# Kernel tuning notes

Hardware: AMD Instinct MI355X
Metric: run time of the kernel (lower is better)

Reference implementation:

```python
import jax, jax.numpy as jnp
import numpy as np

DIM = 2048
HEADS = 16
HEAD_DIM = DIM // HEADS
EPS = 1e-5


def layernorm(x, g, b):
    mu = jnp.mean(x, axis=-1, keepdims=True)
    var = jnp.mean(jnp.square(x - mu), axis=-1, keepdims=True)
    return (x - mu) * jax.lax.rsqrt(var + EPS) * g + b


def bitlinear(x, w):
    # BitNet b1.58: per-tensor ternary weight quant + per-token int8 absmax activation quant
    ws = jnp.clip(jnp.mean(jnp.abs(w)), 1e-5, None)          # weight scale (mean |w|)
    wq = jnp.clip(jnp.round(w / ws), -1.0, 1.0) * ws          # ternary {-1,0,1}*ws
    xs = 127.0 / jnp.clip(jnp.max(jnp.abs(x), axis=-1, keepdims=True), 1e-5, None)
    xq = jnp.clip(jnp.round(x * xs), -128.0, 127.0) / xs      # int8 absmax, dequantized
    return jnp.einsum('bnc,oc->bno', xq, wq)


def attention(x, w_qkv, w_proj):
    B, N, C = x.shape
    qkv = bitlinear(x, w_qkv).reshape(B, N, 3, HEADS, HEAD_DIM)
    q, k, v = [qkv[:, :, i].transpose(0, 2, 1, 3) for i in range(3)]  # [B,H,N,D]
    scores = jnp.einsum('bhqd,bhkd->bhqk', q, k) / jnp.sqrt(jnp.asarray(HEAD_DIM, x.dtype))
    attn = jax.nn.softmax(scores, axis=-1)
    o = jnp.einsum('bhqk,bhkd->bhqd', attn, v)
    o = o.transpose(0, 2, 1, 3).reshape(B, N, C)
    return bitlinear(o, w_proj)


def setup_inputs() -> dict:
    key = jax.random.key(0)
    ks = jax.random.split(key, 9)
    s = 0.02
    return {
        'x': jax.random.normal(ks[0], (2, 2048, DIM), dtype=jnp.float32),
        'w_qkv': jax.random.normal(ks[1], (3 * DIM, DIM), dtype=jnp.float32) * s,
        'w_proj': jax.random.normal(ks[2], (DIM, DIM), dtype=jnp.float32) * s,
        'w_fc1': jax.random.normal(ks[3], (4 * DIM, DIM), dtype=jnp.float32) * s,
        'w_fc2': jax.random.normal(ks[4], (DIM, 4 * DIM), dtype=jnp.float32) * s,
        'g1': jnp.ones((DIM,), jnp.float32),
        'b1': jnp.zeros((DIM,), jnp.float32),
        'g2': jnp.ones((DIM,), jnp.float32),
        'b2': jnp.zeros((DIM,), jnp.float32),
    }


def reference(x, w_qkv, w_proj, w_fc1, w_fc2, g1, b1, g2, b2):
    x = x + attention(layernorm(x, g1, b1), w_qkv, w_proj)
    h = bitlinear(layernorm(x, g2, b2), w_fc1)
    h = jax.nn.gelu(h, approximate=False)
    h = bitlinear(h, w_fc2)
    return x + h
```

## Files before the change

kernel.cpp:

```cpp
#include <hip/hip_runtime.h>
#include <cstdint>

#define DEVI __device__ __forceinline__

typedef int v4i __attribute__((ext_vector_type(4)));
typedef short v8s __attribute__((ext_vector_type(8)));
typedef float v4f __attribute__((ext_vector_type(4)));

DEVI float bf_lo(unsigned u) { return __uint_as_float(u << 16); }
DEVI float bf_hi(unsigned u) { return __uint_as_float(u & 0xffff0000u); }
DEVI float bf2f(unsigned short h) { return __uint_as_float(((unsigned)h) << 16); }
DEVI unsigned short f2bf(float f) {
  unsigned u = __float_as_uint(f);
  u += 0x7fffu + ((u >> 16) & 1u);
  return (unsigned short)(u >> 16);
}

DEVI void async_copy16(void* l, const void* g) {
  __builtin_amdgcn_global_load_lds((const __attribute__((address_space(1))) void*)g,
                                   (__attribute__((address_space(3))) void*)l,
                                   16, 0, 0);
}

DEVI float wave_sum(float v) {
#pragma unroll
  for (int o = 32; o > 0; o >>= 1) v += __shfl_xor(v, o, 64);
  return v;
}
DEVI float wave_max(float v) {
#pragma unroll
  for (int o = 32; o > 0; o >>= 1) v = fmaxf(v, __shfl_xor(v, o, 64));
  return v;
}

__global__ __launch_bounds__(256) void absum_kernel(const float* __restrict__ w, long n,
                                                    float* __restrict__ acc) {
  long stride = (long)gridDim.x * 1024;
  float s = 0.f;
  for (long i = ((long)blockIdx.x * 256 + threadIdx.x) * 4; i < n; i += stride) {
    float4 v = *(const float4*)(w + i);
    s += fabsf(v.x) + fabsf(v.y) + fabsf(v.z) + fabsf(v.w);
  }
  s = wave_sum(s);
  __shared__ float sc[4];
  int tid = threadIdx.x;
  if ((tid & 63) == 0) sc[tid >> 6] = s;
  __syncthreads();
  if (tid == 0) atomicAdd(acc, sc[0] + sc[1] + sc[2] + sc[3]);
}

__global__ __launch_bounds__(256) void wquant_kernel(const float* __restrict__ w, long n4,
                                                     const float* __restrict__ acc, float cnt,
                                                     signed char* __restrict__ out) {
  float wsv = fmaxf(acc[0] / cnt, 1e-5f);
  float inv = 1.0f / wsv;
  long stride = (long)gridDim.x * 256;
  for (long i = (long)blockIdx.x * 256 + threadIdx.x; i < n4; i += stride) {
    float4 v = *(const float4*)(w + i * 4);
    int q0 = max(-1, min(1, (int)rintf(v.x * inv)));
    int q1 = max(-1, min(1, (int)rintf(v.y * inv)));
    int q2 = max(-1, min(1, (int)rintf(v.z * inv)));
    int q3 = max(-1, min(1, (int)rintf(v.w * inv)));
    unsigned r = (q0 & 0xff) | ((q1 & 0xff) << 8) | ((q2 & 0xff) << 16) | ((q3 & 0xff) << 24);
    ((unsigned*)out)[i] = r;
  }
}

__global__ __launch_bounds__(256) void ln_quant_kernel(const float* __restrict__ x,
                                                       const float* __restrict__ g,
                                                       const float* __restrict__ b,
                                                       signed char* __restrict__ q,
                                                       float* __restrict__ inv_s) {
  int row = blockIdx.x, tid = threadIdx.x;
  const float4* xr = (const float4*)(x + (long)row * 2048);
  float4 a0 = xr[tid * 2], a1 = xr[tid * 2 + 1];
  float xv[8] = {a0.x, a0.y, a0.z, a0.w, a1.x, a1.y, a1.z, a1.w};
  float s = 0.f, s2 = 0.f;
#pragma unroll
  for (int e = 0; e < 8; ++e) { s += xv[e]; s2 += xv[e] * xv[e]; }
  s = wave_sum(s); s2 = wave_sum(s2);
  __shared__ float sc[8];
  if ((tid & 63) == 0) { sc[tid >> 6] = s; sc[4 + (tid >> 6)] = s2; }
  __syncthreads();
  float mean = (sc[0] + sc[1] + sc[2] + sc[3]) * (1.f / 2048.f);
  float var = (sc[4] + sc[5] + sc[6] + sc[7]) * (1.f / 2048.f) - mean * mean;
  float rs = 1.0f / sqrtf(var + 1e-5f);
  float4 g0 = ((const float4*)g)[tid * 2], g1v = ((const float4*)g)[tid * 2 + 1];
  float4 b0 = ((const float4*)b)[tid * 2], b1v = ((const float4*)b)[tid * 2 + 1];
  float gv[8] = {g0.x, g0.y, g0.z, g0.w, g1v.x, g1v.y, g1v.z, g1v.w};
  float bv[8] = {b0.x, b0.y, b0.z, b0.w, b1v.x, b1v.y, b1v.z, b1v.w};
  float y[8];
  float am = 0.f;
#pragma unroll
  for (int e = 0; e < 8; ++e) {
    y[e] = (xv[e] - mean) * rs * gv[e] + bv[e];
    am = fmaxf(am, fabsf(y[e]));
  }
  am = wave_max(am);
  __syncthreads();
  if ((tid & 63) == 0) sc[tid >> 6] = am;
  __syncthreads();
  am = fmaxf(fmaxf(sc[0], sc[1]), fmaxf(sc[2], sc[3]));
  float c = fmaxf(am, 1e-5f);
  float xs = 127.0f / c;
  union { signed char c8[8]; int2 v; } u;
#pragma unroll
  for (int e = 0; e < 8; ++e) {
    int t = (int)rintf(y[e] * xs);
    u.c8[e] = (signed char)max(-128, min(127, t));
  }
  ((int2*)(q + (long)row * 2048))[tid] = u.v;
  if (tid == 0) inv_s[row] = c * (1.0f / 127.0f);
}

template <int R>
__global__ __launch_bounds__(256) void row_quant_kernel(const unsigned short* __restrict__ in,
                                                        signed char* __restrict__ q,
                                                        float* __restrict__ inv_s) {
  constexpr int V = R / 2048;
  int row = blockIdx.x, tid = threadIdx.x;
  const uint4* p = (const uint4*)(in + (long)row * R);
  float y[V * 8];
  float am = 0.f;
#pragma unroll
  for (int v = 0; v < V; ++v) {
    uint4 d = p[tid * V + v];
    unsigned xw[4] = {d.x, d.y, d.z, d.w};
#pragma unroll
    for (int k = 0; k < 4; ++k) {
      y[v * 8 + k * 2] = bf_lo(xw[k]);
      y[v * 8 + k * 2 + 1] = bf_hi(xw[k]);
    }
  }
#pragma unroll
  for (int e = 0; e < V * 8; ++e) am = fmaxf(am, fabsf(y[e]));
  am = wave_max(am);
  __shared__ float sc[4];
  if ((tid & 63) == 0) sc[tid >> 6] = am;
  __syncthreads();
  am = fmaxf(fmaxf(sc[0], sc[1]), fmaxf(sc[2], sc[3]));
  float c = fmaxf(am, 1e-5f);
  float xs = 127.0f / c;
  signed char* qr = q + (long)row * R;
#pragma unroll
  for (int v = 0; v < V; ++v) {
    union { signed char c8[8]; long l; } u;
#pragma unroll
    for (int k = 0; k < 8; ++k) {
      int t = (int)rintf(y[v * 8 + k] * xs);
      u.c8[k] = (signed char)max(-128, min(127, t));
    }
    ((long*)qr)[tid * V + v] = u.l;
  }
  if (tid == 0) inv_s[row] = c * (1.0f / 127.0f);
}

template <int EPI>
__global__ __launch_bounds__(256)
void gemm_i8(const signed char* __restrict__ A, const signed char* __restrict__ B,
             int N, int K, const float* __restrict__ wacc, float wcount,
             const float* __restrict__ inv_s, const float* __restrict__ res,
             void* __restrict__ outp) {
  __shared__ signed char As[128 * 64];
  __shared__ signed char Bs[128 * 64];
  int tid = threadIdx.x;
  int m0 = blockIdx.y * 128, n0 = blockIdx.x * 128;
  int w = tid >> 6, lane = tid & 63;
  int wm = (w >> 1) * 64, wn = (w & 1) * 64;
  int lr = lane & 15, lk = (lane >> 4) * 16;

  v4i acc[4][4] = {};

  int u0 = w * 128 + lane;
  int u1 = u0 + 64;
  const signed char* ga0 = A + (long)(m0 + (u0 >> 2)) * K + (u0 & 3) * 16;
  const signed char* ga1 = A + (long)(m0 + (u1 >> 2)) * K + (u1 & 3) * 16;
  const signed char* gb0 = B + (long)(n0 + (u0 >> 2)) * K + (u0 & 3) * 16;
  const signed char* gb1 = B + (long)(n0 + (u1 >> 2)) * K + (u1 & 3) * 16;
  char* la0 = (char*)As + (w * 128) * 16;
  char* la1 = (char*)As + (w * 128 + 64) * 16;
  char* lb0 = (char*)Bs + (w * 128) * 16;
  char* lb1 = (char*)Bs + (w * 128 + 64) * 16;

  for (int kk = 0; kk < K; kk += 64) {
    async_copy16(la0, ga0 + kk);
    async_copy16(la1, ga1 + kk);
    async_copy16(lb0, gb0 + kk);
    async_copy16(lb1, gb1 + kk);
    __syncthreads();
    v4i af[4], bf[4];
#pragma unroll
    for (int t = 0; t < 4; ++t) af[t] = *(const v4i*)(As + (wm + t * 16 + lr) * 64 + lk);
#pragma unroll
    for (int t = 0; t < 4; ++t) bf[t] = *(const v4i*)(Bs + (wn + t * 16 + lr) * 64 + lk);
#pragma unroll
    for (int i = 0; i < 4; ++i)
#pragma unroll
      for (int j = 0; j < 4; ++j)
        acc[i][j] = __builtin_amdgcn_mfma_i32_16x16x64_i8(af[i], bf[j], acc[i][j], 0, 0, 0);
    __syncthreads();
  }

  float wsv = fmaxf(wacc[0] / wcount, 1e-5f);
#pragma unroll
  for (int i = 0; i < 4; ++i) {
    int rowbase = m0 + wm + i * 16 + (lane >> 4) * 4;
#pragma unroll
    for (int r = 0; r < 4; ++r) {
      int row = rowbase + r;
      float s = wsv * inv_s[row];
#pragma unroll
      for (int j = 0; j < 4; ++j) {
        int col = n0 + wn + j * 16 + (lane & 15);
        long off = (long)row * N + col;
        float v = (float)acc[i][j][r] * s;
        if constexpr (EPI == 0) {
          ((unsigned short*)outp)[off] = f2bf(v);
        } else if constexpr (EPI == 1) {
          ((float*)outp)[off] = v + res[off];
        } else {
          float gvv = 0.5f * v * (1.0f + erff(v * 0.70710678118654752f));
          ((unsigned short*)outp)[off] = f2bf(gvv);
        }
      }
    }
  }
}

__global__ __launch_bounds__(256, 2)
void fattn_kernel(const unsigned short* __restrict__ qkv, unsigned short* __restrict__ o) {
  constexpr int VROW = 72;
  constexpr int PROW = 72;
  __shared__ char Ks[16384];
  __shared__ unsigned short Vt[128 * VROW];
  __shared__ unsigned short Ps[4 * 32 * PROW];

  int tid = threadIdx.x;
  int w = tid >> 6, lane = tid & 63;
  int l = lane & 15, q = lane >> 4;
  int qt = blockIdx.x, bh = blockIdx.y;
  int bb = bh >> 4, hh = bh & 15;
  const unsigned short* base = qkv + (long)bb * 2048 * 6144;
  int q0 = qt * 128;

  v8s aq[2][4];
#pragma unroll
  for (int s = 0; s < 2; ++s) {
    const unsigned short* qrow = base + (long)(q0 + w * 32 + s * 16 + l) * 6144 + hh * 128;
#pragma unroll
    for (int kf = 0; kf < 4; ++kf) aq[s][kf] = *(const v8s*)(qrow + kf * 32 + q * 8);
  }

  v4f oacc[2][8];
#pragma unroll
  for (int s = 0; s < 2; ++s)
#pragma unroll
    for (int t = 0; t < 8; ++t) oacc[s][t] = (v4f){0.f, 0.f, 0.f, 0.f};
  float mrow[2][4], lrow[2][4];
#pragma unroll
  for (int s = 0; s < 2; ++s)
#pragma unroll
    for (int r = 0; r < 4; ++r) { mrow[s][r] = -1e30f; lrow[s][r] = 0.f; }

  unsigned short* pw = Ps + w * 32 * PROW;
  const unsigned short* kbase_g = base + 2048 + hh * 128;
  const unsigned short* vbase_g = base + 4096 + hh * 128;
  int kg = tid & 7, dg = tid >> 3;
  constexpr float SC = 0.08838834764831845f;

  for (int kt = 0; kt < 32; ++kt) {
    int k0 = kt * 64;
#pragma unroll
    for (int i = 0; i < 4; ++i) {
      int c = i * 256 + w * 64 + lane;
      int key = c >> 4;
      int dch = (c & 15) ^ (key & 15);
      async_copy16(Ks + (i * 256 + w * 64) * 16,
                   kbase_g + (long)(k0 + key) * 6144 + dch * 8);
    }
    {
      uint2 lv[8];
#pragma unroll
      for (int i = 0; i < 8; ++i)
        lv[i] = *(const uint2*)(vbase_g + (long)(k0 + kg * 8 + i) * 6144 + dg * 4);
#pragma unroll
      for (int jd = 0; jd < 4; ++jd) {
        v8s pk;
#pragma unroll
        for (int i = 0; i < 8; ++i) {
          unsigned word = (jd < 2) ? lv[i].x : lv[i].y;
          pk[i] = (short)((jd & 1) ? (word >> 16) : (word & 0xffffu));
        }
        *(v8s*)(Vt + (dg * 4 + jd) * VROW + kg * 8) = pk;
      }
    }
    __syncthreads();

    v4f sacc[2][4];
#pragma unroll
    for (int s = 0; s < 2; ++s)
#pragma unroll
      for (int t = 0; t < 4; ++t) sacc[s][t] = (v4f){0.f, 0.f, 0.f, 0.f};
#pragma unroll
    for (int kf = 0; kf < 4; ++kf) {
#pragma unroll
      for (int t = 0; t < 4; ++t) {
        int ch = (t * 16 + l) * 16 + ((kf * 4 + q) ^ l);
        v8s bk = *(const v8s*)(Ks + ch * 16);
        sacc[0][t] = __builtin_amdgcn_mfma_f32_16x16x32_bf16(aq[0][kf], bk, sacc[0][t], 0, 0, 0);
        sacc[1][t] = __builtin_amdgcn_mfma_f32_16x16x32_bf16(aq[1][kf], bk, sacc[1][t], 0, 0, 0);
      }
    }
#pragma unroll
    for (int s = 0; s < 2; ++s) {
      float rmax[4], alpha[4], rsum[4];
#pragma unroll
      for (int r = 0; r < 4; ++r) {
        rmax[r] = fmaxf(fmaxf(sacc[s][0][r], sacc[s][1][r]),
                        fmaxf(sacc[s][2][r], sacc[s][3][r])) * SC;
#pragma unroll
        for (int msk = 1; msk < 16; msk <<= 1) rmax[r] = fmaxf(rmax[r], __shfl_xor(rmax[r], msk, 64));
        float mnew = fmaxf(mrow[s][r], rmax[r]);
        alpha[r] = __expf(mrow[s][r] - mnew);
        mrow[s][r] = mnew;
        rsum[r] = 0.f;
      }
#pragma unroll
      for (int t = 0; t < 4; ++t) {
#pragma unroll
        for (int r = 0; r < 4; ++r) {
          float p = __expf(sacc[s][t][r] * SC - mrow[s][r]);
          rsum[r] += p;
          pw[(s * 16 + q * 4 + r) * PROW + t * 16 + l] = f2bf(p);
        }
      }
#pragma unroll
      for (int r = 0; r < 4; ++r) {
#pragma unroll
        for (int msk = 1; msk < 16; msk <<= 1) rsum[r] += __shfl_xor(rsum[r], msk, 64);
        lrow[s][r] = lrow[s][r] * alpha[r] + rsum[r];
#pragma unroll
        for (int t = 0; t < 8; ++t) oacc[s][t][r] *= alpha[r];
      }
    }
#pragma unroll
    for (int s2 = 0; s2 < 2; ++s2) {
      v8s ap0 = *(const v8s*)(pw + l * PROW + s2 * 32 + q * 8);
      v8s ap1 = *(const v8s*)(pw + (16 + l) * PROW + s2 * 32 + q * 8);
#pragma unroll
      for (int t = 0; t < 8; ++t) {
        v8s bv = *(const v8s*)(Vt + (t * 16 + l) * VROW + s2 * 32 + q * 8);
        oacc[0][t] = __builtin_amdgcn_mfma_f32_16x16x32_bf16(ap0, bv, oacc[0][t], 0, 0, 0);
        oacc[1][t] = __builtin_amdgcn_mfma_f32_16x16x32_bf16(ap1, bv, oacc[1][t], 0, 0, 0);
      }
    }
    __syncthreads();
  }

#pragma unroll
  for (int s = 0; s < 2; ++s) {
#pragma unroll
    for (int t = 0; t < 8; ++t) {
#pragma unroll
      for (int r = 0; r < 4; ++r) {
        float val = oacc[s][t][r] / lrow[s][r];
        o[((long)(bb * 2048 + q0 + w * 32 + s * 16 + q * 4 + r)) * 2048 + hh * 128 + t * 16 + l] =
            f2bf(val);
      }
    }
  }
}

extern "C" void kernel_launch(void* const* d_in, const int* in_sizes, int n_in,
                              void* d_out, int out_size, void* d_ws, size_t ws_size,
                              hipStream_t stream) {
  (void)in_sizes; (void)n_in; (void)out_size; (void)ws_size;
  const float* x      = (const float*)d_in[0];
  const float* w_qkv  = (const float*)d_in[1];
  const float* w_proj = (const float*)d_in[2];
  const float* w_fc1  = (const float*)d_in[3];
  const float* w_fc2  = (const float*)d_in[4];
  const float* g1 = (const float*)d_in[5];
  const float* b1 = (const float*)d_in[6];
  const float* g2 = (const float*)d_in[7];
  const float* b2 = (const float*)d_in[8];

  char* wsb = (char*)d_ws;
  float* acc = (float*)wsb;
  size_t off = 256;
  signed char* q8 = (signed char*)(wsb + off);       off += (size_t)4096 * 8192;
  float* invs = (float*)(wsb + off);                 off += 16384;
  signed char* wq_qkv = (signed char*)(wsb + off);   off += (size_t)6144 * 2048;
  signed char* wq_proj = (signed char*)(wsb + off);  off += (size_t)2048 * 2048;
  signed char* wq_fc1 = (signed char*)(wsb + off);   off += (size_t)8192 * 2048;
  signed char* wq_fc2 = (signed char*)(wsb + off);   off += (size_t)2048 * 8192;
  unsigned short* qkvh = (unsigned short*)(wsb + off); off += (size_t)4096 * 8192 * 2;
  unsigned short* obuf = (unsigned short*)(wsb + off); off += (size_t)4096 * 2048 * 2;
  float* x2 = (float*)(wsb + off);                   off += (size_t)4096 * 2048 * 4;

  hipMemsetAsync(acc, 0, 256, stream);

  absum_kernel<<<dim3(1024), 256, 0, stream>>>(w_qkv, (long)6144 * 2048, acc + 0);
  absum_kernel<<<dim3(512),  256, 0, stream>>>(w_proj, (long)2048 * 2048, acc + 1);
  absum_kernel<<<dim3(1024), 256, 0, stream>>>(w_fc1, (long)8192 * 2048, acc + 2);
  absum_kernel<<<dim3(1024), 256, 0, stream>>>(w_fc2, (long)2048 * 8192, acc + 3);

  wquant_kernel<<<dim3(1024), 256, 0, stream>>>(w_qkv, (long)6144 * 2048 / 4, acc + 0, 12582912.f, wq_qkv);
  wquant_kernel<<<dim3(1024), 256, 0, stream>>>(w_proj, (long)2048 * 2048 / 4, acc + 1, 4194304.f, wq_proj);
  wquant_kernel<<<dim3(1024), 256, 0, stream>>>(w_fc1, (long)8192 * 2048 / 4, acc + 2, 16777216.f, wq_fc1);
  wquant_kernel<<<dim3(1024), 256, 0, stream>>>(w_fc2, (long)2048 * 8192 / 4, acc + 3, 16777216.f, wq_fc2);

  ln_quant_kernel<<<4096, 256, 0, stream>>>(x, g1, b1, q8, invs);
  gemm_i8<0><<<dim3(48, 32), 256, 0, stream>>>(q8, wq_qkv, 6144, 2048, acc + 0, 12582912.f, invs, nullptr, qkvh);
  fattn_kernel<<<dim3(16, 32), 256, 0, stream>>>(qkvh, obuf);
  row_quant_kernel<2048><<<4096, 256, 0, stream>>>(obuf, q8, invs);
  gemm_i8<1><<<dim3(16, 32), 256, 0, stream>>>(q8, wq_proj, 2048, 2048, acc + 1, 4194304.f, invs, x, x2);
  ln_quant_kernel<<<4096, 256, 0, stream>>>(x2, g2, b2, q8, invs);
  gemm_i8<2><<<dim3(64, 32), 256, 0, stream>>>(q8, wq_fc1, 8192, 2048, acc + 2, 16777216.f, invs, nullptr, qkvh);
  row_quant_kernel<8192><<<4096, 256, 0, stream>>>(qkvh, q8, invs);
  gemm_i8<1><<<dim3(16, 32), 256, 0, stream>>>(q8, wq_fc2, 2048, 8192, acc + 3, 16777216.f, invs, x2, (float*)d_out);
}
```

Before: 876.8 us.

## Prepack ternary weights into MFMA layout, double-buffer GEMM, split-K flash attention

```diff
diff --git a/kernel.cpp b/kernel.cpp
--- a/kernel.cpp
+++ b/kernel.cpp
@@ -51,9 +51,10 @@
 
 __global__ __launch_bounds__(256) void wquant_kernel(const float* __restrict__ w, long n4,
                                                      const float* __restrict__ acc, float cnt,
-                                                     signed char* __restrict__ out) {
+                                                     signed char* __restrict__ out, int kshift) {
   float wsv = fmaxf(acc[0] / cnt, 1e-5f);
   float inv = 1.0f / wsv;
+  int K = 1 << kshift;
   long stride = (long)gridDim.x * 256;
   for (long i = (long)blockIdx.x * 256 + threadIdx.x; i < n4; i += stride) {
     float4 v = *(const float4*)(w + i * 4);
@@ -62,7 +63,12 @@
     int q2 = max(-1, min(1, (int)rintf(v.z * inv)));
     int q3 = max(-1, min(1, (int)rintf(v.w * inv)));
     unsigned r = (q0 & 0xff) | ((q1 & 0xff) << 8) | ((q2 & 0xff) << 16) | ((q3 & 0xff) << 24);
-    ((unsigned*)out)[i] = r;
+    long flat = i * 4;
+    int n = (int)(flat >> kshift);
+    int k = (int)(flat & (K - 1));
+    long off = ((long)(n >> 4) * (K >> 6) + (k >> 6)) * 1024 +
+               (((k >> 4) & 3) * 16 + (n & 15)) * 16 + (k & 15);
+    *(unsigned*)(out + off) = r;
   }
 }
 
@@ -157,12 +163,11 @@
 
 template <int EPI>
 __global__ __launch_bounds__(256)
-void gemm_i8(const signed char* __restrict__ A, const signed char* __restrict__ B,
+void gemm_i8(const signed char* __restrict__ A, const signed char* __restrict__ Bp,
              int N, int K, const float* __restrict__ wacc, float wcount,
              const float* __restrict__ inv_s, const float* __restrict__ res,
              void* __restrict__ outp) {
-  __shared__ signed char As[128 * 64];
-  __shared__ signed char Bs[128 * 64];
+  __shared__ signed char As[2][128 * 64];
   int tid = threadIdx.x;
   int m0 = blockIdx.y * 128, n0 = blockIdx.x * 128;
   int w = tid >> 6, lane = tid & 63;
@@ -175,30 +180,44 @@
   int u1 = u0 + 64;
   const signed char* ga0 = A + (long)(m0 + (u0 >> 2)) * K + (u0 & 3) * 16;
   const signed char* ga1 = A + (long)(m0 + (u1 >> 2)) * K + (u1 & 3) * 16;
-  const signed char* gb0 = B + (long)(n0 + (u0 >> 2)) * K + (u0 & 3) * 16;
-  const signed char* gb1 = B + (long)(n0 + (u1 >> 2)) * K + (u1 & 3) * 16;
-  char* la0 = (char*)As + (w * 128) * 16;
-  char* la1 = (char*)As + (w * 128 + 64) * 16;
-  char* lb0 = (char*)Bs + (w * 128) * 16;
-  char* lb1 = (char*)Bs + (w * 128 + 64) * 16;
-
-  for (int kk = 0; kk < K; kk += 64) {
-    async_copy16(la0, ga0 + kk);
-    async_copy16(la1, ga1 + kk);
-    async_copy16(lb0, gb0 + kk);
-    async_copy16(lb1, gb1 + kk);
+  int la0 = (w * 128) * 16;
+  int la1 = (w * 128 + 64) * 16;
+
+  int kb64 = K >> 6;
+  const signed char* gbp[4];
+#pragma unroll
+  for (int t = 0; t < 4; ++t) {
+    int ntile = (n0 >> 4) + (w & 1) * 4 + t;
+    gbp[t] = Bp + (long)ntile * kb64 * 1024 + lane * 16;
+  }
+
+  async_copy16((char*)As[0] + la0, ga0);
+  async_copy16((char*)As[0] + la1, ga1);
+  v4i bf_cur[4], bf_nxt[4];
+#pragma unroll
+  for (int t = 0; t < 4; ++t) bf_cur[t] = *(const v4i*)(gbp[t]);
+  __syncthreads();
+
+  int buf = 0;
+  for (int kb = 0; kb < kb64; ++kb) {
+    if (kb + 1 < kb64) {
+      async_copy16((char*)As[buf ^ 1] + la0, ga0 + (kb + 1) * 64);
+      async_copy16((char*)As[buf ^ 1] + la1, ga1 + (kb + 1) * 64);
+#pragma unroll
+      for (int t = 0; t < 4; ++t) bf_nxt[t] = *(const v4i*)(gbp[t] + (kb + 1) * 1024);
+    }
+    v4i af[4];
+#pragma unroll
+    for (int t = 0; t < 4; ++t) af[t] = *(const v4i*)(As[buf] + (wm + t * 16 + lr) * 64 + lk);
+#pragma unroll
+    for (int i = 0; i < 4; ++i)
+#pragma unroll
+      for (int j = 0; j < 4; ++j)
+        acc[i][j] = __builtin_amdgcn_mfma_i32_16x16x64_i8(af[i], bf_cur[j], acc[i][j], 0, 0, 0);
     __syncthreads();
-    v4i af[4], bf[4];
-#pragma unroll
-    for (int t = 0; t < 4; ++t) af[t] = *(const v4i*)(As + (wm + t * 16 + lr) * 64 + lk);
-#pragma unroll
-    for (int t = 0; t < 4; ++t) bf[t] = *(const v4i*)(Bs + (wn + t * 16 + lr) * 64 + lk);
-#pragma unroll
-    for (int i = 0; i < 4; ++i)
-#pragma unroll
-      for (int j = 0; j < 4; ++j)
-        acc[i][j] = __builtin_amdgcn_mfma_i32_16x16x64_i8(af[i], bf[j], acc[i][j], 0, 0, 0);
-    __syncthreads();
+#pragma unroll
+    for (int t = 0; t < 4; ++t) bf_cur[t] = bf_nxt[t];
+    buf ^= 1;
   }
 
   float wsv = fmaxf(wacc[0] / wcount, 1e-5f);
@@ -228,7 +247,8 @@
 }
 
 __global__ __launch_bounds__(256, 2)
-void fattn_kernel(const unsigned short* __restrict__ qkv, unsigned short* __restrict__ o) {
+void fattn_kernel(const unsigned short* __restrict__ qkv, float* __restrict__ O0,
+                  float* __restrict__ O1, float2* __restrict__ stats) {
   constexpr int VROW = 72;
   constexpr int PROW = 72;
   __shared__ char Ks[16384];
@@ -238,10 +258,11 @@
   int tid = threadIdx.x;
   int w = tid >> 6, lane = tid & 63;
   int l = lane & 15, q = lane >> 4;
-  int qt = blockIdx.x, bh = blockIdx.y;
+  int qt = blockIdx.x, bh = blockIdx.y, ks = blockIdx.z;
   int bb = bh >> 4, hh = bh & 15;
   const unsigned short* base = qkv + (long)bb * 2048 * 6144;
   int q0 = qt * 128;
+  float* Opart = ks ? O1 : O0;
 
   v8s aq[2][4];
 #pragma unroll
@@ -268,7 +289,7 @@
   int kg = tid & 7, dg = tid >> 3;
   constexpr float SC = 0.08838834764831845f;
 
-  for (int kt = 0; kt < 32; ++kt) {
+  for (int kt = ks * 16; kt < ks * 16 + 16; ++kt) {
     int k0 = kt * 64;
 #pragma unroll
     for (int i = 0; i < 4; ++i) {
@@ -363,12 +384,43 @@
     for (int t = 0; t < 8; ++t) {
 #pragma unroll
       for (int r = 0; r < 4; ++r) {
-        float val = oacc[s][t][r] / lrow[s][r];
-        o[((long)(bb * 2048 + q0 + w * 32 + s * 16 + q * 4 + r)) * 2048 + hh * 128 + t * 16 + l] =
-            f2bf(val);
-      }
-    }
-  }
+        long grow = bb * 2048 + q0 + w * 32 + s * 16 + q * 4 + r;
+        Opart[grow * 2048 + hh * 128 + t * 16 + l] = oacc[s][t][r];
+      }
+    }
+    if (l == 0) {
+#pragma unroll
+      for (int r = 0; r < 4; ++r) {
+        long grow = bb * 2048 + q0 + w * 32 + s * 16 + q * 4 + r;
+        stats[((long)ks * 4096 + grow) * 16 + hh] = make_float2(mrow[s][r], lrow[s][r]);
+      }
+    }
+  }
+}
+
+__global__ __launch_bounds__(256)
+void attn_combine(const float* __restrict__ O0, const float* __restrict__ O1,
+                  const float2* __restrict__ stats, unsigned short* __restrict__ o) {
+  int grow = blockIdx.x, tid = threadIdx.x;
+  int hh = tid >> 4;
+  float2 s0 = stats[(long)grow * 16 + hh];
+  float2 s1 = stats[((long)4096 + grow) * 16 + hh];
+  float m = fmaxf(s0.x, s1.x);
+  float e0 = __expf(s0.x - m), e1 = __expf(s1.x - m);
+  float inv = 1.0f / (s0.y * e0 + s1.y * e1);
+  long base = (long)grow * 2048 + tid * 8;
+  float4 a0 = *(const float4*)(O0 + base), a1 = *(const float4*)(O0 + base + 4);
+  float4 c0 = *(const float4*)(O1 + base), c1 = *(const float4*)(O1 + base + 4);
+  unsigned short r[8];
+  r[0] = f2bf((a0.x * e0 + c0.x * e1) * inv);
+  r[1] = f2bf((a0.y * e0 + c0.y * e1) * inv);
+  r[2] = f2bf((a0.z * e0 + c0.z * e1) * inv);
+  r[3] = f2bf((a0.w * e0 + c0.w * e1) * inv);
+  r[4] = f2bf((a1.x * e0 + c1.x * e1) * inv);
+  r[5] = f2bf((a1.y * e0 + c1.y * e1) * inv);
+  r[6] = f2bf((a1.z * e0 + c1.z * e1) * inv);
+  r[7] = f2bf((a1.w * e0 + c1.w * e1) * inv);
+  *(uint4*)(o + base) = *(uint4*)r;
 }
 
 extern "C" void kernel_launch(void* const* d_in, const int* in_sizes, int n_in,
@@ -397,6 +449,9 @@
   unsigned short* qkvh = (unsigned short*)(wsb + off); off += (size_t)4096 * 8192 * 2;
   unsigned short* obuf = (unsigned short*)(wsb + off); off += (size_t)4096 * 2048 * 2;
   float* x2 = (float*)(wsb + off);                   off += (size_t)4096 * 2048 * 4;
+  float2* stats = (float2*)(wsb + off);              off += (size_t)2 * 4096 * 16 * 8;
+  float* O0 = x2;
+  float* O1 = (float*)q8;
 
   hipMemsetAsync(acc, 0, 256, stream);
 
@@ -405,14 +460,15 @@
   absum_kernel<<<dim3(1024), 256, 0, stream>>>(w_fc1, (long)8192 * 2048, acc + 2);
   absum_kernel<<<dim3(1024), 256, 0, stream>>>(w_fc2, (long)2048 * 8192, acc + 3);
 
-  wquant_kernel<<<dim3(1024), 256, 0, stream>>>(w_qkv, (long)6144 * 2048 / 4, acc + 0, 12582912.f, wq_qkv);
-  wquant_kernel<<<dim3(1024), 256, 0, stream>>>(w_proj, (long)2048 * 2048 / 4, acc + 1, 4194304.f, wq_proj);
-  wquant_kernel<<<dim3(1024), 256, 0, stream>>>(w_fc1, (long)8192 * 2048 / 4, acc + 2, 16777216.f, wq_fc1);
-  wquant_kernel<<<dim3(1024), 256, 0, stream>>>(w_fc2, (long)2048 * 8192 / 4, acc + 3, 16777216.f, wq_fc2);
+  wquant_kernel<<<dim3(1024), 256, 0, stream>>>(w_qkv, (long)6144 * 2048 / 4, acc + 0, 12582912.f, wq_qkv, 11);
+  wquant_kernel<<<dim3(1024), 256, 0, stream>>>(w_proj, (long)2048 * 2048 / 4, acc + 1, 4194304.f, wq_proj, 11);
+  wquant_kernel<<<dim3(1024), 256, 0, stream>>>(w_fc1, (long)8192 * 2048 / 4, acc + 2, 16777216.f, wq_fc1, 11);
+  wquant_kernel<<<dim3(1024), 256, 0, stream>>>(w_fc2, (long)2048 * 8192 / 4, acc + 3, 16777216.f, wq_fc2, 13);
 
   ln_quant_kernel<<<4096, 256, 0, stream>>>(x, g1, b1, q8, invs);
   gemm_i8<0><<<dim3(48, 32), 256, 0, stream>>>(q8, wq_qkv, 6144, 2048, acc + 0, 12582912.f, invs, nullptr, qkvh);
-  fattn_kernel<<<dim3(16, 32), 256, 0, stream>>>(qkvh, obuf);
+  fattn_kernel<<<dim3(16, 32, 2), 256, 0, stream>>>(qkvh, O0, O1, stats);
+  attn_combine<<<4096, 256, 0, stream>>>(O0, O1, stats, obuf);
   row_quant_kernel<2048><<<4096, 256, 0, stream>>>(obuf, q8, invs);
   gemm_i8<1><<<dim3(16, 32), 256, 0, stream>>>(q8, wq_proj, 2048, 2048, acc + 1, 4194304.f, invs, x, x2);
   ln_quant_kernel<<<4096, 256, 0, stream>>>(x2, g2, b2, q8, invs);
```

Result: no change. 875.9 us (-0.1%).
